# Kernel optimization log

Measured on AMD Instinct MI355X. Metric: run time of the kernel, lower is better.

## Reference

```python
import jax, jax.numpy as jnp
import numpy as np

H = 512  # hidden_size
L = 2    # num_layers


def setup_inputs() -> dict:
    key = jax.random.key(0)
    ks = jax.random.split(key, 10)
    B, S, I = 64, 512, 512
    s = 1.0 / np.sqrt(H)
    def w(k, shape):
        return jax.random.uniform(k, shape, jnp.float32, -s, s)
    return {
        "x": jax.random.normal(ks[0], (B, S, I), jnp.float32),
        "encoder_h": jax.random.normal(ks[1], (B, 2 * H), jnp.float32),
        "Wih_f": w(ks[2], (L, 3 * H, I)),
        "Whh_f": w(ks[3], (L, 3 * H, H)),
        "bih_f": w(ks[4], (L, 3 * H)),
        "bhh_f": w(ks[5], (L, 3 * H)),
        "Wih_b": w(ks[6], (L, 3 * H, I)),
        "Whh_b": w(ks[7], (L, 3 * H, H)),
        "bih_b": w(ks[8], (L, 3 * H)),
        "bhh_b": w(ks[9], (L, 3 * H)),
    }


def _run_direction(seq, h0, Wih, Whh, bih, bhh):
    """Stacked GRU over time. seq: [B,S,I], h0: [B,H]. Returns ([B,S,H], [B,H]).
    Equivalent to the per-timestep stacked-layer loop in the torch module: each
    layer consumes the previous layer's output stream and its own previous hidden."""
    h_last = h0
    for j in range(L):
        # Precompute input-side gates for the whole sequence (one big GEMM).
        gi = jnp.einsum('bsi,gi->bsg', seq, Wih[j]) + bih[j]  # [B,S,3H]
        Whh_j, bhh_j = Whh[j], bhh[j]

        def step(h, gi_t):
            gh = h @ Whh_j.T + bhh_j                 # [B,3H]
            i_r, i_z, i_n = jnp.split(gi_t, 3, axis=-1)
            h_r, h_z, h_n = jnp.split(gh, 3, axis=-1)
            r = jax.nn.sigmoid(i_r + h_r)
            z = jax.nn.sigmoid(i_z + h_z)
            n = jnp.tanh(i_n + r * h_n)
            h_new = (1.0 - z) * n + z * h
            return h_new, h_new

        h_last, outs = jax.lax.scan(step, h0, jnp.swapaxes(gi, 0, 1))  # outs: [S,B,H]
        seq = jnp.swapaxes(outs, 0, 1)  # [B,S,H] feeds next layer
    return seq, h_last


def reference(x, encoder_h, Wih_f, Whh_f, bih_f, bhh_f, Wih_b, Whh_b, bih_b, bhh_b):
    h0_f = encoder_h[:, :H]
    h0_b = encoder_h[:, H:]
    out_f, h_f = _run_direction(x, h0_f, Wih_f, Whh_f, bih_f, bhh_f)
    x_rev = jnp.flip(x, axis=1)
    out_b_rev, h_b = _run_direction(x_rev, h0_b, Wih_b, Whh_b, bih_b, bhh_b)
    out_b = jnp.flip(out_b_rev, axis=1)
    out = jnp.concatenate([out_f, out_b], axis=2)   # [B,S,2H]
    h = jnp.concatenate([h_f, h_b], axis=1)         # [B,2H]
    return out, h
```

## Files before the change

### kernel.cpp

```cpp
#include <hip/hip_runtime.h>


#define B_ 64
#define S_ 512
#define H_ 512
#define G3_ 1536

typedef __attribute__((ext_vector_type(8))) __bf16 bf16x8;
typedef __attribute__((ext_vector_type(8))) short short8;
typedef __attribute__((ext_vector_type(2))) unsigned long long ull2;
typedef __attribute__((ext_vector_type(4))) float f32x4;
typedef unsigned long long ull;

__device__ __forceinline__ unsigned short f2b(float f) {
  union { float f; unsigned int i; } v; v.f = f;
  unsigned int x = v.i;
  return (unsigned short)((x + 0x7fffu + ((x >> 16) & 1u)) >> 16);
}
__device__ __forceinline__ bf16x8 load8(const unsigned short* p) {
  short8 s = *(const short8*)p;
  return __builtin_bit_cast(bf16x8, s);
}
__device__ __forceinline__ bf16x8 load8f(const float* p) {
  f32x4 a = *(const f32x4*)p, b = *(const f32x4*)(p + 4);
  short8 s;
  s[0] = (short)f2b(a[0]); s[1] = (short)f2b(a[1]);
  s[2] = (short)f2b(a[2]); s[3] = (short)f2b(a[3]);
  s[4] = (short)f2b(b[0]); s[5] = (short)f2b(b[1]);
  s[6] = (short)f2b(b[2]); s[7] = (short)f2b(b[3]);
  return __builtin_bit_cast(bf16x8, s);
}
__device__ __forceinline__ f32x4 mfma16(bf16x8 a, bf16x8 b, f32x4 c) {
  return __builtin_amdgcn_mfma_f32_16x16x32_bf16(a, b, c, 0, 0, 0);
}
__device__ __forceinline__ float sigmoidf_(float x) {
  float e = __expf(-fabsf(x));
  float s = e / (1.0f + e);
  return x >= 0.0f ? 1.0f - s : s;
}
__device__ __forceinline__ float tanhf_(float x) {
  float e = __expf(-2.0f * fabsf(x));
  float r = (1.0f - e) / (1.0f + e);
  return x >= 0.0f ? r : -r;
}
__device__ __forceinline__ bf16x8 load16a(ull* p) {
  ull2 v;
  v[0] = __hip_atomic_load(p, __ATOMIC_RELAXED, __HIP_MEMORY_SCOPE_AGENT);
  v[1] = __hip_atomic_load(p + 1, __ATOMIC_RELAXED, __HIP_MEMORY_SCOPE_AGENT);
  return __builtin_bit_cast(bf16x8, v);
}
__device__ __forceinline__ bf16x8 load16p(const ull* p) {
  ull2 v = *(const ull2*)p;
  return __builtin_bit_cast(bf16x8, v);
}
__device__ __forceinline__ ull pack4(const float* f) {
  ull v = 0;
#pragma unroll
  for (int j = 0; j < 4; ++j) v |= (ull)f2b(f[j]) << (16 * j);
  return v;
}

__global__ void cvt_x(const float* __restrict__ x, ull* __restrict__ xc) {
  int i = blockIdx.x * 256 + threadIdx.x;
  int b = i & 63, cell = (i >> 6) & 63, txx = i >> 12;
  const float* src = x + ((size_t)b * 512 + txx) * 512 + cell * 8;
  float s0[4] = {src[0], src[1], src[2], src[3]};
  float s1[4] = {src[4], src[5], src[6], src[7]};
  size_t o = ((size_t)txx * 4096 + cell * 64 + b) * 2;
  xc[o]     = pack4(s0);
  xc[o + 1] = pack4(s1);
}

__global__ void init_ring(const float* __restrict__ enc, ull* __restrict__ ring) {
  int i = blockIdx.x * 256 + threadIdx.x;
  if (i >= 32768) return;
  int ld = i >> 13;
  int d = ld & 1;
  int rest = i & 8191;
  int half = rest & 1, b = (rest >> 1) & 63, cell = rest >> 7;
  const float* e = enc + (size_t)b * 1024 + d * 512 + cell * 8 + half * 4;
  float s[4] = {e[0], e[1], e[2], e[3]};
  ring[(size_t)ld * 65536 + 7 * 8192 + rest] = pack4(s);
}

__global__ __launch_bounds__(256) void gru_fused(
    const float* __restrict__ x,
    const ull* __restrict__ xc, int usexc,
    const float* __restrict__ enc,
    const float* __restrict__ WihF, const float* __restrict__ WihB,
    const float* __restrict__ WhhF, const float* __restrict__ WhhB,
    const float* __restrict__ bihF, const float* __restrict__ bihB,
    const float* __restrict__ bhhF, const float* __restrict__ bhhB,
    ull* __restrict__ ring,
    unsigned int* __restrict__ flags,
    float* __restrict__ dout) {
  __shared__ __align__(16) unsigned short wih2[24576];
  __shared__ __align__(16) unsigned short whh2[24576];
  __shared__ float hpub[64 * 20];
  __shared__ int lcnt[8];

  const int tid = threadIdx.x;
  const int lane = tid & 63;
  const int wv = tid >> 6;
  const int wg = (int)blockIdx.x;
  const int l = wg >> 6, d = (wg >> 5) & 1, cb = wg & 31;
  const int colbase = cb * 16;
  const int rowA = lane & 15, kb = lane >> 4;

  const float* Wih = (d ? WihB : WihF) + (size_t)l * G3_ * H_;
  const float* Whh = (d ? WhhB : WhhF) + (size_t)l * G3_ * H_;
  const float* bi = (d ? bihB : bihF) + l * G3_;
  const float* bh = (d ? bhhB : bhhF) + l * G3_;

  if (tid < 8) lcnt[tid] = 0;
  for (int i = tid; i < 3072; i += 256) {
    int gate = i >> 10;
    int rest = i & 1023;
    int kk = rest >> 6;
    int l6 = rest & 63;
    int c = l6 & 15, k = l6 >> 4;
    size_t gro = (size_t)(gate * 512 + colbase + c) * 512 + kk * 32 + k * 8;
    *(short8*)&wih2[i * 8] = __builtin_bit_cast(short8, load8f(Wih + gro));
    *(short8*)&whh2[i * 8] = __builtin_bit_cast(short8, load8f(Whh + gro));
  }
  __syncthreads();

  const int col16 = rowA;
  const int hc = colbase + col16;
  const float brz_r = bi[hc] + bh[hc];
  const float brz_z = bi[512 + hc] + bh[512 + hc];
  const float bi_n = bi[1024 + hc];
  const float bh_n = bh[1024 + hc];

  const int bq = wv * 16 + kb * 4;
  const int arow = wv * 16 + rowA;

  float hm[4];
#pragma unroll
  for (int rg = 0; rg < 4; ++rg)
    hm[rg] = enc[(size_t)(bq + rg) * 1024 + d * 512 + hc];

  unsigned int* fl0 = flags + d * (32 * 32);
  unsigned int* fl1 = flags + (2 + d) * (32 * 32);
  unsigned int* flo = flags + (l * 2 + d) * (32 * 32);
  ull* ring0 = ring + (size_t)d * 65536;
  ull* ringl = ring + (size_t)(l * 2 + d) * 65536;

  const int prow = wv * 16 + (lane >> 2);
  const int pcellL = (lane >> 1) & 1;
  const int phalf = lane & 1;
  const int pc0 = pcellL * 8 + phalf * 4;
  const int pidx = ((2 * cb + pcellL) * 64 + prow) * 2 + phalf;

  for (int t = 0; t < 512; ++t) {
    bf16x8 aIn[16];
    if (l == 0) {
      int txx = d ? (511 - t) : t;
      if (usexc) {
        const ull* xp = xc + (size_t)txx * 8192;
#pragma unroll
        for (int kk = 0; kk < 16; ++kk)
          aIn[kk] = load16p(xp + (size_t)((kk * 4 + kb) * 64 + arow) * 2);
      } else {
        const float* ap = x + ((size_t)arow * 512 + txx) * 512 + kb * 8;
#pragma unroll
        for (int kk = 0; kk < 16; ++kk) aIn[kk] = load8f(ap + kk * 32);
      }
    }

    {
      const int needA = (l == 0) ? t : (t + 1);
      const int needB = (l == 0) ? (t - 7) : t;
      unsigned int* watch;
      int need;
      if (lane < 32) { watch = fl0 + lane * 32;        need = needA; }
      else           { watch = fl1 + (lane - 32) * 32; need = needB; }
      if (need > 0) {
        while (__hip_atomic_load(watch, __ATOMIC_RELAXED,
                                 __HIP_MEMORY_SCOPE_AGENT) < (unsigned)need) {}
      }
    }
    asm volatile("" ::: "memory");

    if (l == 1) {
      ull* rp = ring0 + (size_t)(t & 7) * 8192;
#pragma unroll
      for (int kk = 0; kk < 16; ++kk)
        aIn[kk] = load16a(rp + (size_t)((kk * 4 + kb) * 64 + arow) * 2);
    }
    ull* rpo = ringl + (size_t)((t + 7) & 7) * 8192;
    bf16x8 aOwn[16];
#pragma unroll
    for (int kk = 0; kk < 16; ++kk)
      aOwn[kk] = load16a(rpo + (size_t)((kk * 4 + kb) * 64 + arow) * 2);

    f32x4 accr = {0,0,0,0}, accz = {0,0,0,0}, acni = {0,0,0,0}, acnh = {0,0,0,0};
#pragma unroll
    for (int kk = 0; kk < 16; ++kk) {
      const int o = kk * 512 + lane * 8;
      accr = mfma16(aIn[kk],  load8(&wih2[o]), accr);
      accr = mfma16(aOwn[kk], load8(&whh2[o]), accr);
      accz = mfma16(aIn[kk],  load8(&wih2[8192 + o]), accz);
      accz = mfma16(aOwn[kk], load8(&whh2[8192 + o]), accz);
      acni = mfma16(aIn[kk],  load8(&wih2[16384 + o]), acni);
      acnh = mfma16(aOwn[kk], load8(&whh2[16384 + o]), acnh);
    }

#pragma unroll
    for (int rg = 0; rg < 4; ++rg) {
      float r = sigmoidf_(accr[rg] + brz_r);
      float z = sigmoidf_(accz[rg] + brz_z);
      float n = tanhf_(acni[rg] + bi_n + r * (acnh[rg] + bh_n));
      float hnew = (1.0f - z) * n + z * hm[rg];
      hm[rg] = hnew;
      hpub[(bq + rg) * 20 + col16] = hnew;
    }
    asm volatile("" ::: "memory");

    {
      f32x4 v4 = *(f32x4*)&hpub[prow * 20 + pc0];
      float s[4] = {v4[0], v4[1], v4[2], v4[3]};
      __hip_atomic_store(ringl + (size_t)(t & 7) * 8192 + pidx, pack4(s),
                         __ATOMIC_RELAXED, __HIP_MEMORY_SCOPE_AGENT);
    }
    asm volatile("s_waitcnt vmcnt(0)" ::: "memory");

    if (lane == 0) {
      int old = atomicAdd(&lcnt[t & 7], 1);
      if (old == 3) {
        lcnt[t & 7] = 0;
        __hip_atomic_store(flo + cb * 32, (unsigned)(t + 1),
                           __ATOMIC_RELAXED, __HIP_MEMORY_SCOPE_AGENT);
      }
    }

    if (l == 1) {
      const int tox = d ? (511 - t) : t;
#pragma unroll
      for (int rg = 0; rg < 4; ++rg)
        dout[((size_t)(bq + rg) * 512 + tox) * 1024 + d * 512 + hc] = hm[rg];
    }
  }
}

__global__ void h_epi(float* __restrict__ dout) {
  int i = blockIdx.x * 256 + threadIdx.x;
  if (i >= B_ * 2 * H_) return;
  int b = i >> 10, j = i & 1023;
  int t = (j < H_) ? (S_ - 1) : 0;
  dout[(size_t)B_ * S_ * 2 * H_ + i] = dout[((size_t)b * S_ + t) * (2 * H_) + j];
}

extern "C" void kernel_launch(void* const* d_in, const int* in_sizes, int n_in,
                              void* d_out, int out_size, void* d_ws, size_t ws_size,
                              hipStream_t stream) {
  const float* x    = (const float*)d_in[0];
  const float* enc  = (const float*)d_in[1];
  const float* WihF = (const float*)d_in[2];
  const float* WhhF = (const float*)d_in[3];
  const float* bihF = (const float*)d_in[4];
  const float* bhhF = (const float*)d_in[5];
  const float* WihB = (const float*)d_in[6];
  const float* WhhB = (const float*)d_in[7];
  const float* bihB = (const float*)d_in[8];
  const float* bhhB = (const float*)d_in[9];
  float* out = (float*)d_out;

  char* ws = (char*)d_ws;
  unsigned int* flags = (unsigned int*)ws;
  ull* ring  = (ull*)(ws + 65536);
  ull* xc    = (ull*)(ws + 65536 + 2097152);
  const int usexc = (ws_size >= (size_t)65536 + 2097152 + 33554432) ? 1 : 0;

  (void)hipMemsetAsync(flags, 0, 16384, stream);
  if (usexc) cvt_x<<<8192, 256, 0, stream>>>(x, xc);
  init_ring<<<128, 256, 0, stream>>>(enc, ring);
  gru_fused<<<128, 256, 0, stream>>>(x, xc, usexc, enc,
                                     WihF, WihB, WhhF, WhhB,
                                     bihF, bihB, bhhF, bhhB,
                                     ring, flags, out);
  h_epi<<<256, 256, 0, stream>>>(out);
}
```

Before: 2.778 ms.

## Split batch into two independent halves across twice as many workgroups

```diff
diff --git a/kernel.cpp b/kernel.cpp
--- a/kernel.cpp
+++ b/kernel.cpp
@@ -74,16 +74,16 @@
 __global__ void init_ring(const float* __restrict__ enc, ull* __restrict__ ring) {
   int i = blockIdx.x * 256 + threadIdx.x;
   if (i >= 32768) return;
-  int ld = i >> 13;
-  int d = ld & 1;
-  int rest = i & 8191;
-  int half = rest & 1, b = (rest >> 1) & 63, cell = rest >> 7;
-  const float* e = enc + (size_t)b * 1024 + d * 512 + cell * 8 + half * 4;
+  int gid = i >> 12;
+  int u = i & 4095;
+  int d = (gid >> 1) & 1, beta = gid & 1;
+  int half = u & 1, b = (u >> 1) & 31, cell = u >> 6;
+  const float* e = enc + (size_t)(beta * 32 + b) * 1024 + d * 512 + cell * 8 + half * 4;
   float s[4] = {e[0], e[1], e[2], e[3]};
-  ring[(size_t)ld * 65536 + 7 * 8192 + rest] = pack4(s);
-}
-
-__global__ __launch_bounds__(256) void gru_fused(
+  ring[(size_t)gid * 32768 + 7 * 4096 + u] = pack4(s);
+}
+
+__global__ __launch_bounds__(128) void gru_fused(
     const float* __restrict__ x,
     const ull* __restrict__ xc, int usexc,
     const float* __restrict__ enc,
@@ -96,14 +96,17 @@
     float* __restrict__ dout) {
   __shared__ __align__(16) unsigned short wih2[24576];
   __shared__ __align__(16) unsigned short whh2[24576];
-  __shared__ float hpub[64 * 20];
+  __shared__ float hpub[32 * 20];
   __shared__ int lcnt[8];
 
   const int tid = threadIdx.x;
   const int lane = tid & 63;
   const int wv = tid >> 6;
   const int wg = (int)blockIdx.x;
-  const int l = wg >> 6, d = (wg >> 5) & 1, cb = wg & 31;
+  const int l = wg >> 7, d = (wg >> 6) & 1, beta = (wg >> 5) & 1, cb = wg & 31;
+  const int gid = ((l * 2 + d) << 1) | beta;
+  const int gidA = gid & 3;
+  const int gidB = gidA | 4;
   const int colbase = cb * 16;
   const int rowA = lane & 15, kb = lane >> 4;
 
@@ -113,7 +116,7 @@
   const float* bh = (d ? bhhB : bhhF) + l * G3_;
 
   if (tid < 8) lcnt[tid] = 0;
-  for (int i = tid; i < 3072; i += 256) {
+  for (int i = tid; i < 3072; i += 128) {
     int gate = i >> 10;
     int rest = i & 1023;
     int kk = rest >> 6;
@@ -138,19 +141,19 @@
   float hm[4];
 #pragma unroll
   for (int rg = 0; rg < 4; ++rg)
-    hm[rg] = enc[(size_t)(bq + rg) * 1024 + d * 512 + hc];
-
-  unsigned int* fl0 = flags + d * (32 * 32);
-  unsigned int* fl1 = flags + (2 + d) * (32 * 32);
-  unsigned int* flo = flags + (l * 2 + d) * (32 * 32);
-  ull* ring0 = ring + (size_t)d * 65536;
-  ull* ringl = ring + (size_t)(l * 2 + d) * 65536;
-
-  const int prow = wv * 16 + (lane >> 2);
-  const int pcellL = (lane >> 1) & 1;
-  const int phalf = lane & 1;
+    hm[rg] = enc[(size_t)(beta * 32 + bq + rg) * 1024 + d * 512 + hc];
+
+  unsigned int* flA = flags + gidA * 1024;
+  unsigned int* flB = flags + gidB * 1024;
+  unsigned int* flo = flags + gid * 1024;
+  ull* ringA = ring + (size_t)gidA * 32768;
+  ull* ringl = ring + (size_t)gid * 32768;
+
+  const int pb = tid >> 2;
+  const int pq = tid & 3;
+  const int pcellL = pq >> 1, phalf = pq & 1;
   const int pc0 = pcellL * 8 + phalf * 4;
-  const int pidx = ((2 * cb + pcellL) * 64 + prow) * 2 + phalf;
+  const int pidx = ((2 * cb + pcellL) * 32 + pb) * 2 + phalf;
 
   for (int t = 0; t < 512; ++t) {
     bf16x8 aIn[16];
@@ -160,9 +163,9 @@
         const ull* xp = xc + (size_t)txx * 8192;
 #pragma unroll
         for (int kk = 0; kk < 16; ++kk)
-          aIn[kk] = load16p(xp + (size_t)((kk * 4 + kb) * 64 + arow) * 2);
+          aIn[kk] = load16p(xp + (size_t)((kk * 4 + kb) * 64 + beta * 32 + arow) * 2);
       } else {
-        const float* ap = x + ((size_t)arow * 512 + txx) * 512 + kb * 8;
+        const float* ap = x + ((size_t)(beta * 32 + arow) * 512 + txx) * 512 + kb * 8;
 #pragma unroll
         for (int kk = 0; kk < 16; ++kk) aIn[kk] = load8f(ap + kk * 32);
       }
@@ -173,8 +176,8 @@
       const int needB = (l == 0) ? (t - 7) : t;
       unsigned int* watch;
       int need;
-      if (lane < 32) { watch = fl0 + lane * 32;        need = needA; }
-      else           { watch = fl1 + (lane - 32) * 32; need = needB; }
+      if (lane < 32) { watch = flA + lane * 32;        need = needA; }
+      else           { watch = flB + (lane - 32) * 32; need = needB; }
       if (need > 0) {
         while (__hip_atomic_load(watch, __ATOMIC_RELAXED,
                                  __HIP_MEMORY_SCOPE_AGENT) < (unsigned)need) {}
@@ -183,16 +186,16 @@
     asm volatile("" ::: "memory");
 
     if (l == 1) {
-      ull* rp = ring0 + (size_t)(t & 7) * 8192;
+      ull* rp = ringA + (size_t)(t & 7) * 4096;
 #pragma unroll
       for (int kk = 0; kk < 16; ++kk)
-        aIn[kk] = load16a(rp + (size_t)((kk * 4 + kb) * 64 + arow) * 2);
-    }
-    ull* rpo = ringl + (size_t)((t + 7) & 7) * 8192;
+        aIn[kk] = load16a(rp + (size_t)((kk * 4 + kb) * 32 + arow) * 2);
+    }
+    ull* rpo = ringl + (size_t)((t + 7) & 7) * 4096;
     bf16x8 aOwn[16];
 #pragma unroll
     for (int kk = 0; kk < 16; ++kk)
-      aOwn[kk] = load16a(rpo + (size_t)((kk * 4 + kb) * 64 + arow) * 2);
+      aOwn[kk] = load16a(rpo + (size_t)((kk * 4 + kb) * 32 + arow) * 2);
 
     f32x4 accr = {0,0,0,0}, accz = {0,0,0,0}, acni = {0,0,0,0}, acnh = {0,0,0,0};
 #pragma unroll
@@ -218,16 +221,16 @@
     asm volatile("" ::: "memory");
 
     {
-      f32x4 v4 = *(f32x4*)&hpub[prow * 20 + pc0];
+      f32x4 v4 = *(f32x4*)&hpub[pb * 20 + pc0];
       float s[4] = {v4[0], v4[1], v4[2], v4[3]};
-      __hip_atomic_store(ringl + (size_t)(t & 7) * 8192 + pidx, pack4(s),
+      __hip_atomic_store(ringl + (size_t)(t & 7) * 4096 + pidx, pack4(s),
                          __ATOMIC_RELAXED, __HIP_MEMORY_SCOPE_AGENT);
     }
     asm volatile("s_waitcnt vmcnt(0)" ::: "memory");
 
     if (lane == 0) {
       int old = atomicAdd(&lcnt[t & 7], 1);
-      if (old == 3) {
+      if (old == 1) {
         lcnt[t & 7] = 0;
         __hip_atomic_store(flo + cb * 32, (unsigned)(t + 1),
                            __ATOMIC_RELAXED, __HIP_MEMORY_SCOPE_AGENT);
@@ -238,7 +241,7 @@
       const int tox = d ? (511 - t) : t;
 #pragma unroll
       for (int rg = 0; rg < 4; ++rg)
-        dout[((size_t)(bq + rg) * 512 + tox) * 1024 + d * 512 + hc] = hm[rg];
+        dout[((size_t)(beta * 32 + bq + rg) * 512 + tox) * 1024 + d * 512 + hc] = hm[rg];
     }
   }
 }
@@ -272,10 +275,10 @@
   ull* xc    = (ull*)(ws + 65536 + 2097152);
   const int usexc = (ws_size >= (size_t)65536 + 2097152 + 33554432) ? 1 : 0;
 
-  (void)hipMemsetAsync(flags, 0, 16384, stream);
+  (void)hipMemsetAsync(flags, 0, 32768, stream);
   if (usexc) cvt_x<<<8192, 256, 0, stream>>>(x, xc);
   init_ring<<<128, 256, 0, stream>>>(enc, ring);
-  gru_fused<<<128, 256, 0, stream>>>(x, xc, usexc, enc,
+  gru_fused<<<256, 128, 0, stream>>>(x, xc, usexc, enc,
                                      WihF, WihB, WhhF, WhhB,
                                      bihF, bihB, bhhF, bhhB,
                                      ring, flags, out);
```

Measured after the change: 2.319 ms (median of 2 runs). 16.5% less time.
